# Optimization experiments

Measured on AMD Instinct MI355X. Metric: run time of the kernel, lower is better.

Reference implementation:

```python
import jax, jax.numpy as jnp
import numpy as np

N, L, D, ZD, H, C = 128, 256, 256, 128, 8, 32
EPS = 1e-5

def _ln(x, w, b):
    mu = jnp.mean(x, axis=-1, keepdims=True)
    var = jnp.var(x, axis=-1, keepdims=True)
    return (x - mu) * jax.lax.rsqrt(var + EPS) * w + b

def setup_inputs() -> dict:
    key = jax.random.key(0)
    ks = jax.random.split(key, 10)
    s = 0.02
    return {
        "m": jax.random.normal(ks[0], (N, L, D), jnp.float32),
        "z": jax.random.normal(ks[1], (L, L, ZD), jnp.float32),
        "ln1_w": jnp.ones((D,), jnp.float32),
        "ln1_b": jnp.zeros((D,), jnp.float32),
        "wq": jax.random.normal(ks[2], (D, H * C), jnp.float32) * s,
        "wk": jax.random.normal(ks[3], (D, H * C), jnp.float32) * s,
        "wv": jax.random.normal(ks[4], (D, H * C), jnp.float32) * s,
        "lnz_w": jnp.ones((ZD,), jnp.float32),
        "lnz_b": jnp.zeros((ZD,), jnp.float32),
        "wz": jax.random.normal(ks[5], (ZD, H), jnp.float32) * s,
        "wg": jax.random.normal(ks[6], (D, H * C), jnp.float32) * s,
        "bg": jnp.zeros((H * C,), jnp.float32),
        "wo": jax.random.normal(ks[7], (H * C, D), jnp.float32) * s,
        "bo": jnp.zeros((D,), jnp.float32),
    }

def reference(m, z, ln1_w, ln1_b, wq, wk, wv, lnz_w, lnz_b, wz, wg, bg, wo, bo):
    mn = _ln(m, ln1_w, ln1_b)                        # [N,L,D]
    q = (mn @ wq).reshape(N, L, H, C)
    k = (mn @ wk).reshape(N, L, H, C)
    v = (mn @ wv).reshape(N, L, H, C)
    b = _ln(z, lnz_w, lnz_b) @ wz                    # [L,L,H] pair bias
    g = jax.nn.sigmoid(mn @ wg + bg).reshape(N, L, H, C)
    att = jnp.einsum('nqhc,nkhc->nqkh', q, k) * (1.0 / np.sqrt(C)) + b[None]
    att = jax.nn.softmax(att, axis=2)                # over key dim
    o = jnp.einsum('nqkh,nkhc->nqhc', att, v) * g    # gated output
    return o.reshape(N, L, H * C) @ wo + bo          # [N,L,D]
```

## Files before the change

kernel.cpp:

```cpp
#include <hip/hip_runtime.h>
#include <math.h>

typedef unsigned short u16;
typedef unsigned int   u32;
typedef __attribute__((ext_vector_type(8)))  short          bf16x8;
typedef __attribute__((ext_vector_type(4)))  short          bf16x4;
typedef __attribute__((ext_vector_type(4)))  float          f32x4;
typedef __attribute__((ext_vector_type(16))) unsigned short u16x16;

static constexpr int Nn = 128;
static constexpr int Ln = 256;
static constexpr int Dn = 256;
static constexpr int ZDn = 128;
static constexpr int Hn = 8;
static constexpr int Cn = 32;
static constexpr int Mrows = Nn * Ln;
static constexpr float EPS = 1e-5f;
static constexpr float LOG2E = 1.4426950408889634f;
static constexpr int HS = 32768 * 32;

__device__ __forceinline__ float bf_s(u16 u)  { union { u32 i; float f; } x; x.i = ((u32)u) << 16; return x.f; }
__device__ __forceinline__ float bf_lo(u32 u) { union { u32 i; float f; } x; x.i = u << 16;         return x.f; }
__device__ __forceinline__ float bf_hi(u32 u) { union { u32 i; float f; } x; x.i = u & 0xffff0000u; return x.f; }
__device__ __forceinline__ u32 fbits(float f) { union { float f; u32 i; } x; x.f = f; return x.i; }
__device__ __forceinline__ u32 f2bf(float f) {
  const u32 i = fbits(f);
  return (i + 0x7fffu + ((i >> 16) & 1u)) >> 16;
}
__device__ __forceinline__ u32 pk2(float a, float b) { return f2bf(a) | (f2bf(b) << 16); }
__device__ __forceinline__ u32 pk2_trunc(float a, float b) {
  return (fbits(b) & 0xffff0000u) | (fbits(a) >> 16);
}

__device__ __forceinline__ f32x4 mfma16(bf16x4 a, bf16x4 b, f32x4 c) {
#if __has_builtin(__builtin_amdgcn_mfma_f32_16x16x16bf16_1k)
  return __builtin_amdgcn_mfma_f32_16x16x16bf16_1k(a, b, c, 0, 0, 0);
#else
  f32x4 d;
  asm volatile("v_mfma_f32_16x16x16_bf16 %0, %1, %2, %3"
               : "=v"(d) : "v"(a), "v"(b), "v"(c));
  return d;
#endif
}

__global__ __launch_bounds__(256) void ln_m_kernel(
    const float* __restrict__ x, const float* __restrict__ w,
    const float* __restrict__ b, u16* __restrict__ y)
{
  const int wave = threadIdx.x >> 6;
  const int lane = threadIdx.x & 63;
  const size_t row = (size_t)blockIdx.x * 4 + wave;
  const float4 xv = ((const float4*)(x + row * Dn))[lane];
  float s  = xv.x + xv.y + xv.z + xv.w;
  float s2 = xv.x*xv.x + xv.y*xv.y + xv.z*xv.z + xv.w*xv.w;
  #pragma unroll
  for (int off = 32; off; off >>= 1) {
    s  += __shfl_xor(s, off);
    s2 += __shfl_xor(s2, off);
  }
  const float mu = s * (1.0f / Dn);
  float var = s2 * (1.0f / Dn) - mu * mu;
  var = fmaxf(var, 0.0f);
  const float rstd = rsqrtf(var + EPS);
  const float4 wv = ((const float4*)w)[lane];
  const float4 bv = ((const float4*)b)[lane];
  float4 yv;
  yv.x = (xv.x - mu) * rstd * wv.x + bv.x;
  yv.y = (xv.y - mu) * rstd * wv.y + bv.y;
  yv.z = (xv.z - mu) * rstd * wv.z + bv.z;
  yv.w = (xv.w - mu) * rstd * wv.w + bv.w;
  uint2 p;
  p.x = pk2(yv.x, yv.y);
  p.y = pk2(yv.z, yv.w);
  ((uint2*)(y + row * Dn))[lane] = p;
}

__global__ __launch_bounds__(256) void wcvt_kernel(
    const float* __restrict__ wq, const float* __restrict__ wk,
    const float* __restrict__ wv, const float* __restrict__ wg,
    const float* __restrict__ wo,
    const float* __restrict__ lnz_w, const float* __restrict__ lnz_b,
    const float* __restrict__ wz,
    u16* __restrict__ wcatT, u16* __restrict__ woTh, u16* __restrict__ woTl,
    float* __restrict__ wkhT, float* __restrict__ Sv, float* __restrict__ bsv)
{
  __shared__ float lds[128][8];
  const int bid = blockIdx.x;
  const int t = threadIdx.x;
  if (bid < 1024) {
    const int n = bid & 255, proj = bid >> 8;
    const float* W = proj == 0 ? wq : proj == 1 ? wk : proj == 2 ? wv : wg;
    float v = W[(size_t)t * 256 + n];
    if (proj == 0) v *= 0.17677669529663687f * LOG2E;
    wcatT[(size_t)bid * 256 + t] = (u16)f2bf(v);
  } else if (bid < 1280) {
    const int n = bid - 1024;
    const float x = wo[(size_t)t * 256 + n];
    const u16 h16 = (u16)f2bf(x);
    woTh[(size_t)n * 256 + t] = h16;
    woTl[(size_t)n * 256 + t] = (u16)f2bf(x - bf_s(h16));
  } else {
    if (t < 128) {
      #pragma unroll
      for (int h = 0; h < 8; ++h) {
        const float v = lnz_w[t] * wz[t * 8 + h];
        lds[t][h] = v;
        wkhT[h * 128 + t] = v;
      }
    }
    __syncthreads();
    if (t < 8) {
      float S = 0.0f, bs = 0.0f;
      for (int k = 0; k < 128; ++k) {
        S  += lds[k][t];
        bs += lnz_b[k] * wz[k * 8 + t];
      }
      Sv[t] = S; bsv[t] = LOG2E * bs;
    }
  }
}

__global__ __launch_bounds__(256) void zbias_kernel(
    const float* __restrict__ z, const float* __restrict__ wkhT,
    const float* __restrict__ Sv, const float* __restrict__ bsv,
    float* __restrict__ b2)
{
  __shared__ float zs[64][132];
  __shared__ float wkT_s[8 * 132];
  __shared__ float mu_s[64], rs_s[64];
  const int t = threadIdx.x;
  const int r0 = blockIdx.x * 64;

  #pragma unroll
  for (int u = 0; u < 8; ++u) {
    const int i = u * 256 + t;
    const int row = i >> 5, c4 = i & 31;
    *(float4*)&zs[row][c4 * 4] =
        *(const float4*)(z + (size_t)(r0 + row) * 128 + c4 * 4);
  }
  #pragma unroll
  for (int u = 0; u < 4; ++u) {
    const int i = u * 256 + t;
    wkT_s[(i >> 7) * 132 + (i & 127)] = wkhT[i];
  }
  __syncthreads();

  {
    const int row = t >> 2, q = t & 3;
    float s = 0.0f, s2 = 0.0f;
    #pragma unroll
    for (int u = 0; u < 8; ++u) {
      const float4 v = *(const float4*)&zs[row][(q * 8 + u) * 4];
      s  += v.x + v.y + v.z + v.w;
      s2 += v.x*v.x + v.y*v.y + v.z*v.z + v.w*v.w;
    }
    s += __shfl_xor(s, 1); s2 += __shfl_xor(s2, 1);
    s += __shfl_xor(s, 2); s2 += __shfl_xor(s2, 2);
    if (q == 0) {
      const float mu = s * (1.0f / 128.0f);
      float var = s2 * (1.0f / 128.0f) - mu * mu;
      var = fmaxf(var, 0.0f);
      mu_s[row] = mu;
      rs_s[row] = rsqrtf(var + EPS);
    }
  }
  __syncthreads();

  {
    const int row = t >> 2, hp = t & 3;
    const int h0 = 2 * hp, h1 = 2 * hp + 1;
    float a0 = 0.0f, a1 = 0.0f;
    #pragma unroll
    for (int c4 = 0; c4 < 32; ++c4) {
      const float4 v  = *(const float4*)&zs[row][c4 * 4];
      const float4 w0 = *(const float4*)&wkT_s[h0 * 132 + c4 * 4];
      const float4 w1 = *(const float4*)&wkT_s[h1 * 132 + c4 * 4];
      a0 = fmaf(v.x, w0.x, a0); a0 = fmaf(v.y, w0.y, a0);
      a0 = fmaf(v.z, w0.z, a0); a0 = fmaf(v.w, w0.w, a0);
      a1 = fmaf(v.x, w1.x, a1); a1 = fmaf(v.y, w1.y, a1);
      a1 = fmaf(v.z, w1.z, a1); a1 = fmaf(v.w, w1.w, a1);
    }
    const float mu = mu_s[row];
    const float rs = rs_s[row] * LOG2E;
    const size_t rg = (size_t)(r0 + row);
    b2[(size_t)h0 * 65536 + rg] = rs * (a0 - mu * Sv[h0]) + bsv[h0];
    b2[(size_t)h1 * 65536 + rg] = rs * (a1 - mu * Sv[h1]) + bsv[h1];
  }
}

__global__ __launch_bounds__(512) void mfma_gemm_qkvg(
    const u16* __restrict__ A, const u16* __restrict__ BT,
    u16* __restrict__ qb, u16* __restrict__ kb,
    u16* __restrict__ vb, u16* __restrict__ gb,
    const float* __restrict__ bg)
{
  __shared__ u16 A_s[128 * 32];
  __shared__ u16 B_s[256 * 32];
  const int t  = threadIdx.x;
  const int w  = t >> 6;
  const int lane = t & 63;
  const int g  = lane >> 4;
  const int li = lane & 15;
  const int m0 = blockIdx.x * 128;
  const int n0 = blockIdx.y * 256;
  const int wr = (w & 1) * 64;
  const int wc = (w >> 1) * 64;

  const f32x4 zf = {0.f, 0.f, 0.f, 0.f};
  f32x4 acc[4][4];
  #pragma unroll
  for (int i = 0; i < 4; ++i)
    #pragma unroll
    for (int j = 0; j < 4; ++j) acc[i][j] = zf;

  for (int k0 = 0; k0 < 256; k0 += 32) {
    __syncthreads();
    {
      const int cb  = w * 1024 + lane * 16;
      const int row = cb >> 6;
      const int ku  = (cb & 63) >> 1;
      __builtin_amdgcn_global_load_lds(
          (const __attribute__((address_space(1))) void*)
              (A + (size_t)(m0 + row) * 256 + k0 + ku),
          (__attribute__((address_space(3))) void*)(A_s + w * 512),
          16, 0, 0);
    }
    #pragma unroll
    for (int i = 0; i < 2; ++i) {
      const int c   = i*8 + w;
      const int cb  = c * 1024 + lane * 16;
      const int row = cb >> 6;
      const int ku  = (cb & 63) >> 1;
      __builtin_amdgcn_global_load_lds(
          (const __attribute__((address_space(1))) void*)
              (BT + (size_t)(n0 + row) * 256 + k0 + ku),
          (__attribute__((address_space(3))) void*)(B_s + c * 512),
          16, 0, 0);
    }
    __syncthreads();
    bf16x8 af[4], bfr[4];
    #pragma unroll
    for (int i = 0; i < 4; ++i)
      af[i] = *(const bf16x8*)&A_s[(wr + i*16 + li) * 32 + g*8];
    #pragma unroll
    for (int j = 0; j < 4; ++j)
      bfr[j] = *(const bf16x8*)&B_s[(wc + j*16 + li) * 32 + g*8];
    #pragma unroll
    for (int i = 0; i < 4; ++i)
      #pragma unroll
      for (int j = 0; j < 4; ++j)
        acc[i][j] = __builtin_amdgcn_mfma_f32_16x16x32_bf16(af[i], bfr[j], acc[i][j], 0, 0, 0);
  }

  #pragma unroll
  for (int j = 0; j < 4; ++j) {
    const int nglob = n0 + wc + j*16 + li;
    const int proj = nglob >> 8;
    const int h    = (nglob >> 5) & 7;
    const int c    = nglob & 31;
    u16* base = proj == 0 ? qb : proj == 1 ? kb : proj == 2 ? vb : gb;
    const float gbias = (proj == 3) ? bg[h*32 + c] : 0.0f;
    #pragma unroll
    for (int i = 0; i < 4; ++i)
      #pragma unroll
      for (int r = 0; r < 4; ++r) {
        const int m = m0 + wr + i*16 + g*4 + r;
        const float v = acc[i][j][r] + gbias;
        base[(size_t)h * HS + (size_t)m * 32 + c] = (u16)f2bf(v);
      }
  }
}

__global__ __launch_bounds__(512) void attn_mfma_kernel(
    const u16* __restrict__ qb, const u16* __restrict__ kb,
    const u16* __restrict__ vb, const u16* __restrict__ gb,
    const float* __restrict__ b2, u16* __restrict__ obuf)
{
  __shared__ u16 VT_s[32 * 264];
  __shared__ u16 K_s[256 * 40];

  const int h = blockIdx.x;
  const int n = blockIdx.y;
  const int t = threadIdx.x;
  const int w = t >> 6;
  const int lane = t & 63;
  const int g  = lane >> 4;
  const int li = lane & 15;
  const size_t hb = (size_t)h * HS;
  const size_t rowb = (size_t)n * 256;

  {
    const int row = t >> 1;
    const int cc  = (t & 1) * 16;
    const uint4* kg = (const uint4*)(kb + hb + (rowb + row) * 32 + cc);
    *(uint4*)&K_s[row * 40 + cc]     = kg[0];
    *(uint4*)&K_s[row * 40 + cc + 8] = kg[1];
    const u16x16 v = *(const u16x16*)(vb + hb + (rowb + row) * 32 + cc);
    #pragma unroll
    for (int c = 0; c < 16; ++c)
      VT_s[(cc + c) * 264 + row] = v[c];
  }

  bf16x8 qfrag[2];
  #pragma unroll
  for (int qt = 0; qt < 2; ++qt)
    qfrag[qt] = *(const bf16x8*)(qb + hb + (rowb + w*32 + qt*16 + li) * 32 + g*8);

  __syncthreads();

  const f32x4 zf = {0.f, 0.f, 0.f, 0.f};
  const bf16x4 ONES = {(short)0x3F80, (short)0x3F80, (short)0x3F80, (short)0x3F80};
  f32x4 oacc[2][2];
  f32x4 lacc[2];
  oacc[0][0] = zf; oacc[0][1] = zf; oacc[1][0] = zf; oacc[1][1] = zf;
  lacc[0] = zf; lacc[1] = zf;

  #pragma unroll 4
  for (int kt = 0; kt < 16; ++kt) {
    const bf16x8 kfrag = *(const bf16x8*)&K_s[(kt*16 + li) * 40 + g*8];
    const bf16x4 vf0 = *(const bf16x4*)&VT_s[(li)      * 264 + kt*16 + g*4];
    const bf16x4 vf1 = *(const bf16x4*)&VT_s[(16 + li) * 264 + kt*16 + g*4];
    #pragma unroll
    for (int qt = 0; qt < 2; ++qt) {
      f32x4 s = __builtin_amdgcn_mfma_f32_16x16x32_bf16(kfrag, qfrag[qt], zf, 0, 0, 0);
      const int q = w*32 + qt*16 + li;
      const float4 b4 = *(const float4*)(b2 + ((size_t)h << 16) +
                                         (size_t)q * 256 + kt*16 + g*4);
      const float p0 = __builtin_amdgcn_exp2f(s[0] + b4.x);
      const float p1 = __builtin_amdgcn_exp2f(s[1] + b4.y);
      const float p2 = __builtin_amdgcn_exp2f(s[2] + b4.z);
      const float p3 = __builtin_amdgcn_exp2f(s[3] + b4.w);
      union { uint2 u; bf16x4 v; } pc;
      pc.u.x = pk2_trunc(p0, p1);
      pc.u.y = pk2_trunc(p2, p3);
      oacc[qt][0] = mfma16(vf0, pc.v, oacc[qt][0]);
      oacc[qt][1] = mfma16(vf1, pc.v, oacc[qt][1]);
      lacc[qt]    = mfma16(ONES, pc.v, lacc[qt]);
    }
  }

  float linv[2];
  linv[0] = 1.0f / lacc[0][0];
  linv[1] = 1.0f / lacc[1][0];

  #pragma unroll
  for (int qt = 0; qt < 2; ++qt) {
    const int q = w*32 + qt*16 + li;
    #pragma unroll
    for (int ct = 0; ct < 2; ++ct) {
      const int c0 = ct*16 + g*4;
      const uint2 gp = *(const uint2*)(gb + hb + (rowb + q) * 32 + c0);
      const float g0 = 1.0f / (1.0f + __expf(-bf_lo(gp.x)));
      const float g1 = 1.0f / (1.0f + __expf(-bf_hi(gp.x)));
      const float g2 = 1.0f / (1.0f + __expf(-bf_lo(gp.y)));
      const float g3 = 1.0f / (1.0f + __expf(-bf_hi(gp.y)));
      uint2 r;
      r.x = pk2(oacc[qt][ct][0] * linv[qt] * g0,
                oacc[qt][ct][1] * linv[qt] * g1);
      r.y = pk2(oacc[qt][ct][2] * linv[qt] * g2,
                oacc[qt][ct][3] * linv[qt] * g3);
      *(uint2*)(obuf + (rowb + q) * 256 + h*32 + c0) = r;
    }
  }
}

__global__ __launch_bounds__(256) void out_proj_kernel(
    const u16* __restrict__ Abuf, const u16* __restrict__ woT,
    const float* __restrict__ bo, float* __restrict__ out)
{
  __shared__ u16 A_s[64 * 264];
  __shared__ u16 B_s[256 * 40];
  const int t  = threadIdx.x;
  const int w  = t >> 6;
  const int lane = t & 63;
  const int g  = lane >> 4;
  const int li = lane & 15;
  const int m0 = blockIdx.x * 64;
  const int wr = (w & 1) * 32;
  const int wc = (w >> 1) * 128;

  #pragma unroll
  for (int j = 0; j < 8; ++j) {
    const int u = j * 256 + t;
    const int row = u >> 5, c8 = u & 31;
    *(uint4*)&A_s[row * 264 + c8 * 8] =
        *(const uint4*)(Abuf + (size_t)(m0 + row) * 256 + c8 * 8);
  }

  const f32x4 zf = {0.f, 0.f, 0.f, 0.f};
  f32x4 acc[2][8];
  #pragma unroll
  for (int i = 0; i < 2; ++i)
    #pragma unroll
    for (int j = 0; j < 8; ++j) acc[i][j] = zf;

  for (int k0 = 0; k0 < 256; k0 += 32) {
    __syncthreads();
    {
      const u16* sh = woT + (size_t)t * 256 + k0;
      #pragma unroll
      for (int u = 0; u < 4; ++u)
        *(uint4*)&B_s[t * 40 + u*8] = *(const uint4*)(sh + u*8);
    }
    __syncthreads();
    bf16x8 af[2];
    #pragma unroll
    for (int i = 0; i < 2; ++i)
      af[i] = *(const bf16x8*)&A_s[(wr + i*16 + li) * 264 + k0 + g*8];
    #pragma unroll
    for (int j = 0; j < 8; ++j) {
      const bf16x8 bfr = *(const bf16x8*)&B_s[(wc + j*16 + li) * 40 + g*8];
      #pragma unroll
      for (int i = 0; i < 2; ++i)
        acc[i][j] = __builtin_amdgcn_mfma_f32_16x16x32_bf16(af[i], bfr, acc[i][j], 0, 0, 0);
    }
  }

  #pragma unroll
  for (int j = 0; j < 8; ++j) {
    const int col = wc + j*16 + li;
    const float bias = bo[col];
    #pragma unroll
    for (int i = 0; i < 2; ++i)
      #pragma unroll
      for (int r = 0; r < 4; ++r) {
        const int m = m0 + wr + i*16 + g*4 + r;
        out[(size_t)m * 256 + col] = acc[i][j][r] + bias;
      }
  }
}

extern "C" void kernel_launch(void* const* d_in, const int* in_sizes, int n_in,
                              void* d_out, int out_size, void* d_ws, size_t ws_size,
                              hipStream_t stream)
{
  const float* m     = (const float*)d_in[0];
  const float* z     = (const float*)d_in[1];
  const float* ln1_w = (const float*)d_in[2];
  const float* ln1_b = (const float*)d_in[3];
  const float* wq    = (const float*)d_in[4];
  const float* wk    = (const float*)d_in[5];
  const float* wv    = (const float*)d_in[6];
  const float* lnz_w = (const float*)d_in[7];
  const float* lnz_b = (const float*)d_in[8];
  const float* wz    = (const float*)d_in[9];
  const float* wg    = (const float*)d_in[10];
  const float* bg    = (const float*)d_in[11];
  const float* wo    = (const float*)d_in[12];
  const float* bo    = (const float*)d_in[13];
  float* out = (float*)d_out;

  char* ws = (char*)d_ws;
  const size_t MB = 1024 * 1024;
  u16*   mn    = (u16*)(ws);
  u16*   qb    = (u16*)(ws + 16*MB);
  u16*   kb    = (u16*)(ws + 32*MB);
  u16*   vb    = (u16*)(ws + 48*MB);
  u16*   gb    = (u16*)(ws + 64*MB);
  float* b2    = (float*)(ws + 80*MB);
  u16*   wcatT = (u16*)(ws + 82*MB);
  u16*   woTh  = (u16*)(ws + 82*MB + 512*1024);
  u16*   woTl  = (u16*)(ws + 82*MB + 640*1024);
  float* wkhT  = (float*)(ws + 82*MB + 768*1024);
  float* Sv    = (float*)(ws + 82*MB + 772*1024);
  float* bsv   = (float*)(ws + 82*MB + 773*1024);
  u16*   obuf  = mn;

  wcvt_kernel<<<1281, 256, 0, stream>>>(wq, wk, wv, wg, wo, lnz_w, lnz_b, wz,
                                        wcatT, woTh, woTl, wkhT, Sv, bsv);
  ln_m_kernel<<<Mrows/4, 256, 0, stream>>>(m, ln1_w, ln1_b, mn);
  zbias_kernel<<<(Ln*Ln)/64, 256, 0, stream>>>(z, wkhT, Sv, bsv, b2);

  mfma_gemm_qkvg<<<dim3(Mrows/128, 1024/256), 512, 0, stream>>>(
      mn, wcatT, qb, kb, vb, gb, bg);

  attn_mfma_kernel<<<dim3(Hn, Nn), 512, 0, stream>>>(qb, kb, vb, gb, b2, obuf);

  out_proj_kernel<<<Mrows/64, 256, 0, stream>>>(obuf, woTh, bo, out);
}
```

Measured before the change: 121.2 us.

## Retile output projection with direct-to-LDS loads and fold bias into MFMA

The output projection moves from 64-row tiles with 256 threads to 128-row tiles with 512 threads, each wave computing a 64x64 tile. Both A and the transposed weight are streamed per k-slice straight into LDS with global_load_lds, replacing the full-row A preload and register-staged B copy. The attention kernel now passes the pair bias in as the MFMA accumulator instead of adding it afterwards, and pads the transposed V buffer to stride 268 to change the LDS bank pattern. The unpadded 32-wide LDS rows in the projection may cause bank conflicts on fragment reads.

```diff
diff --git a/kernel.cpp b/kernel.cpp
--- a/kernel.cpp
+++ b/kernel.cpp
@@ -18,6 +18,7 @@
 static constexpr float EPS = 1e-5f;
 static constexpr float LOG2E = 1.4426950408889634f;
 static constexpr int HS = 32768 * 32;
+static constexpr int VTS = 268;
 
 __device__ __forceinline__ float bf_s(u16 u)  { union { u32 i; float f; } x; x.i = ((u32)u) << 16; return x.f; }
 __device__ __forceinline__ float bf_lo(u32 u) { union { u32 i; float f; } x; x.i = u << 16;         return x.f; }
@@ -276,7 +277,7 @@
     const u16* __restrict__ vb, const u16* __restrict__ gb,
     const float* __restrict__ b2, u16* __restrict__ obuf)
 {
-  __shared__ u16 VT_s[32 * 264];
+  __shared__ u16 VT_s[32 * VTS];
   __shared__ u16 K_s[256 * 40];
 
   const int h = blockIdx.x;
@@ -298,7 +299,7 @@
     const u16x16 v = *(const u16x16*)(vb + hb + (rowb + row) * 32 + cc);
     #pragma unroll
     for (int c = 0; c < 16; ++c)
-      VT_s[(cc + c) * 264 + row] = v[c];
+      VT_s[(cc + c) * VTS + row] = v[c];
   }
 
   bf16x8 qfrag[2];
@@ -318,18 +319,19 @@
   #pragma unroll 4
   for (int kt = 0; kt < 16; ++kt) {
     const bf16x8 kfrag = *(const bf16x8*)&K_s[(kt*16 + li) * 40 + g*8];
-    const bf16x4 vf0 = *(const bf16x4*)&VT_s[(li)      * 264 + kt*16 + g*4];
-    const bf16x4 vf1 = *(const bf16x4*)&VT_s[(16 + li) * 264 + kt*16 + g*4];
+    const bf16x4 vf0 = *(const bf16x4*)&VT_s[(li)      * VTS + kt*16 + g*4];
+    const bf16x4 vf1 = *(const bf16x4*)&VT_s[(16 + li) * VTS + kt*16 + g*4];
     #pragma unroll
     for (int qt = 0; qt < 2; ++qt) {
-      f32x4 s = __builtin_amdgcn_mfma_f32_16x16x32_bf16(kfrag, qfrag[qt], zf, 0, 0, 0);
       const int q = w*32 + qt*16 + li;
-      const float4 b4 = *(const float4*)(b2 + ((size_t)h << 16) +
-                                         (size_t)q * 256 + kt*16 + g*4);
-      const float p0 = __builtin_amdgcn_exp2f(s[0] + b4.x);
-      const float p1 = __builtin_amdgcn_exp2f(s[1] + b4.y);
-      const float p2 = __builtin_amdgcn_exp2f(s[2] + b4.z);
-      const float p3 = __builtin_amdgcn_exp2f(s[3] + b4.w);
+      const f32x4 bias4 = *(const f32x4*)(b2 + ((size_t)h << 16) +
+                                          (size_t)q * 256 + kt*16 + g*4);
+      const f32x4 s = __builtin_amdgcn_mfma_f32_16x16x32_bf16(
+          kfrag, qfrag[qt], bias4, 0, 0, 0);
+      const float p0 = __builtin_amdgcn_exp2f(s[0]);
+      const float p1 = __builtin_amdgcn_exp2f(s[1]);
+      const float p2 = __builtin_amdgcn_exp2f(s[2]);
+      const float p3 = __builtin_amdgcn_exp2f(s[3]);
       union { uint2 u; bf16x4 v; } pc;
       pc.u.x = pk2_trunc(p0, p1);
       pc.u.y = pk2_trunc(p2, p3);
@@ -364,64 +366,73 @@
   }
 }
 
-__global__ __launch_bounds__(256) void out_proj_kernel(
+__global__ __launch_bounds__(512) void out_proj_kernel(
     const u16* __restrict__ Abuf, const u16* __restrict__ woT,
     const float* __restrict__ bo, float* __restrict__ out)
 {
-  __shared__ u16 A_s[64 * 264];
-  __shared__ u16 B_s[256 * 40];
+  __shared__ u16 A_s[128 * 32];
+  __shared__ u16 B_s[256 * 32];
   const int t  = threadIdx.x;
   const int w  = t >> 6;
   const int lane = t & 63;
   const int g  = lane >> 4;
   const int li = lane & 15;
-  const int m0 = blockIdx.x * 64;
-  const int wr = (w & 1) * 32;
-  const int wc = (w >> 1) * 128;
-
-  #pragma unroll
-  for (int j = 0; j < 8; ++j) {
-    const int u = j * 256 + t;
-    const int row = u >> 5, c8 = u & 31;
-    *(uint4*)&A_s[row * 264 + c8 * 8] =
-        *(const uint4*)(Abuf + (size_t)(m0 + row) * 256 + c8 * 8);
-  }
+  const int m0 = blockIdx.x * 128;
+  const int wr = (w & 1) * 64;
+  const int wc = (w >> 1) * 64;
 
   const f32x4 zf = {0.f, 0.f, 0.f, 0.f};
-  f32x4 acc[2][8];
-  #pragma unroll
-  for (int i = 0; i < 2; ++i)
-    #pragma unroll
-    for (int j = 0; j < 8; ++j) acc[i][j] = zf;
+  f32x4 acc[4][4];
+  #pragma unroll
+  for (int i = 0; i < 4; ++i)
+    #pragma unroll
+    for (int j = 0; j < 4; ++j) acc[i][j] = zf;
 
   for (int k0 = 0; k0 < 256; k0 += 32) {
     __syncthreads();
     {
-      const u16* sh = woT + (size_t)t * 256 + k0;
+      const int cb  = w * 1024 + lane * 16;
+      const int row = cb >> 6;
+      const int ku  = (cb & 63) >> 1;
+      __builtin_amdgcn_global_load_lds(
+          (const __attribute__((address_space(1))) void*)
+              (Abuf + (size_t)(m0 + row) * 256 + k0 + ku),
+          (__attribute__((address_space(3))) void*)(A_s + w * 512),
+          16, 0, 0);
+    }
+    #pragma unroll
+    for (int i = 0; i < 2; ++i) {
+      const int c   = i*8 + w;
+      const int cb  = c * 1024 + lane * 16;
+      const int row = cb >> 6;
+      const int ku  = (cb & 63) >> 1;
+      __builtin_amdgcn_global_load_lds(
+          (const __attribute__((address_space(1))) void*)
+              (woT + (size_t)row * 256 + k0 + ku),
+          (__attribute__((address_space(3))) void*)(B_s + c * 512),
+          16, 0, 0);
+    }
+    __syncthreads();
+    bf16x8 af[4], bfr[4];
+    #pragma unroll
+    for (int i = 0; i < 4; ++i)
+      af[i] = *(const bf16x8*)&A_s[(wr + i*16 + li) * 32 + g*8];
+    #pragma unroll
+    for (int j = 0; j < 4; ++j)
+      bfr[j] = *(const bf16x8*)&B_s[(wc + j*16 + li) * 32 + g*8];
+    #pragma unroll
+    for (int i = 0; i < 4; ++i)
       #pragma unroll
-      for (int u = 0; u < 4; ++u)
-        *(uint4*)&B_s[t * 40 + u*8] = *(const uint4*)(sh + u*8);
-    }
-    __syncthreads();
-    bf16x8 af[2];
-    #pragma unroll
-    for (int i = 0; i < 2; ++i)
-      af[i] = *(const bf16x8*)&A_s[(wr + i*16 + li) * 264 + k0 + g*8];
-    #pragma unroll
-    for (int j = 0; j < 8; ++j) {
-      const bf16x8 bfr = *(const bf16x8*)&B_s[(wc + j*16 + li) * 40 + g*8];
-      #pragma unroll
-      for (int i = 0; i < 2; ++i)
-        acc[i][j] = __builtin_amdgcn_mfma_f32_16x16x32_bf16(af[i], bfr, acc[i][j], 0, 0, 0);
-    }
-  }
-
-  #pragma unroll
-  for (int j = 0; j < 8; ++j) {
+      for (int j = 0; j < 4; ++j)
+        acc[i][j] = __builtin_amdgcn_mfma_f32_16x16x32_bf16(af[i], bfr[j], acc[i][j], 0, 0, 0);
+  }
+
+  #pragma unroll
+  for (int j = 0; j < 4; ++j) {
     const int col = wc + j*16 + li;
     const float bias = bo[col];
     #pragma unroll
-    for (int i = 0; i < 2; ++i)
+    for (int i = 0; i < 4; ++i)
       #pragma unroll
       for (int r = 0; r < 4; ++r) {
         const int m = m0 + wr + i*16 + g*4 + r;
@@ -476,5 +487,5 @@
 
   attn_mfma_kernel<<<dim3(Hn, Nn), 512, 0, stream>>>(qb, kb, vb, gb, b2, obuf);
 
-  out_proj_kernel<<<Mrows/64, 256, 0, stream>>>(obuf, woTh, bo, out);
-}
+  out_proj_kernel<<<Mrows/128, 512, 0, stream>>>(obuf, woTh, bo, out);
+}
```

Result: faster. 115.1 us (-5.0%).
